# Kernel optimization log

Measured on AMD Instinct MI355X. Metric: run time of the kernel, lower is better.

## Reference

```python
import jax, jax.numpy as jnp
import numpy as np

B, H, D = 8, 2048, 2
K_COUPLE = 1.0
DT = 1.0
ALPHA_SCALE = 1.0


def setup_inputs() -> dict:
    key = jax.random.key(0)
    k1, k2, k3, k4, k5 = jax.random.split(key, 5)
    theta_prev = jax.random.normal(k1, (B, H, D), dtype=jnp.float32)
    gamma = jax.random.normal(k2, (B, H), dtype=jnp.float32)
    A = jax.random.uniform(k3, (B, H, H), dtype=jnp.float32)
    omega = jax.random.normal(k4, (H, D), dtype=jnp.float32) * 0.1
    kappa = jnp.ones((H, D), dtype=jnp.float32)
    direction_learner = jax.random.normal(k5, (H, H), dtype=jnp.float32) * 0.01
    return {"theta_prev": theta_prev, "gamma": gamma, "A": A,
            "omega": omega, "kappa": kappa, "direction_learner": direction_learner}


def reference(theta_prev, gamma, A, omega, kappa, direction_learner):
    b, h, d = theta_prev.shape
    # Symmetrized, positive lateral connectivity
    A_lat = 0.5 * (A + jnp.swapaxes(A, 1, 2))
    A_lat = jax.nn.relu(A_lat) + 1e-6  # [B,H,H]
    # OT surrogate: normalized cost, antisymmetric learned direction -> phase lag alpha
    cost = 1.0 / A_lat
    c_min = jnp.min(cost, axis=(1, 2), keepdims=True)
    c_max = jnp.max(cost, axis=(1, 2), keepdims=True)
    norm_cost = (cost - c_min) / (c_max - c_min + 1e-6)
    direction_mask = jnp.tanh(direction_learner - direction_learner.T)  # [H,H]
    alpha = (ALPHA_SCALE * direction_mask[None, :, :] * norm_cost)[..., None]  # [B,H,H,1]
    # Pairwise phase interaction: sum_j A_ij * sin(theta_j - theta_i - alpha_ij)
    theta_i = theta_prev[:, :, None, :]  # [B,H,1,D]
    theta_j = theta_prev[:, None, :, :]  # [B,1,H,D]
    phase_diff = theta_j - theta_i - alpha  # [B,H,H,D]
    interaction = jnp.sum(A_lat[..., None] * jnp.sin(phase_diff), axis=2)  # [B,H,D]
    coupling = (K_COUPLE / float(h)) * interaction
    drive = kappa * jnp.sin(gamma[..., None] - theta_prev)
    theta_dot = omega + coupling + drive
    return theta_prev + DT * theta_dot
```

## Files before the change

### kernel.cpp

```cpp
#include <hip/hip_runtime.h>
#include <hip/hip_fp16.h>

#define B 8
#define H 2048
#define D 2
#define HH (H*H)
#define TILE 64
#define NT (H/TILE)
#define NPAIR (NT*(NT+1)/2)
#define NJC 8
#define JC (H/NJC)
#define WJ (JC/4)
#define SUB 16
#define NSUB (WJ/SUB)
#define INV2PI 0.15915494309189535f

__device__ __forceinline__ float fsin(float x) { return __builtin_amdgcn_sinf(x * INV2PI); }
__device__ __forceinline__ float fcos(float x) { return __builtin_amdgcn_cosf(x * INV2PI); }


__global__ __launch_bounds__(256) void k_dmpre(
    const float* __restrict__ dl, __half* __restrict__ dm,
    const float* __restrict__ theta, const float* __restrict__ gamma,
    const float* __restrict__ omega, const float* __restrict__ kappa,
    float* __restrict__ out, float4* __restrict__ sc) {
    int ti = blockIdx.x, tj = blockIdx.y;
    int t = threadIdx.x, c = t & 63, r0 = t >> 6;
    __shared__ float l2[TILE][TILE + 1];

    float v[16];
    #pragma unroll
    for (int k = 0; k < 16; k++)
        v[k] = dl[(size_t)(tj * TILE + r0 + 4 * k) * H + ti * TILE + c];
    #pragma unroll
    for (int k = 0; k < 16; k++) l2[r0 + 4 * k][c] = v[k];
    __syncthreads();
    #pragma unroll
    for (int k = 0; k < 16; k++)
        v[k] = dl[(size_t)(ti * TILE + r0 + 4 * k) * H + tj * TILE + c];
    #pragma unroll
    for (int k = 0; k < 16; k++) {
        int il = r0 + 4 * k;
        float x = v[k] - l2[c][il];
        float x2 = x * x;
        float w = x * fmaf(x2, fmaf(x2, 0.13333334f, -0.33333334f), 1.0f);
        dm[(size_t)(ti * TILE + il) * H + tj * TILE + c] = __float2half(w);
    }

    int bid = blockIdx.y * NT + blockIdx.x;
    if (bid < (B * H) / 256) {
        int g = bid * 256 + t;
        int i = g & (H - 1);
        float th0 = theta[(size_t)g * 2 + 0];
        float th1 = theta[(size_t)g * 2 + 1];
        sc[g] = make_float4(fsin(th0), fcos(th0), fsin(th1), fcos(th1));
        float gm = gamma[g];
        out[(size_t)g * 2 + 0] = th0 + omega[i * 2 + 0] + kappa[i * 2 + 0] * fsin(gm - th0);
        out[(size_t)g * 2 + 1] = th1 + omega[i * 2 + 1] + kappa[i * 2 + 1] * fsin(gm - th1);
    }
}

__global__ __launch_bounds__(256) void k_minmax(const float* __restrict__ A,
                                                float* __restrict__ pmn,
                                                float* __restrict__ pmx) {
    int b = blockIdx.y;
    int tp = blockIdx.x;
    int pid = b * NPAIR + tp;
    int ti = 0;
    while (tp >= NT - ti) { tp -= NT - ti; ti++; }
    int tj = ti + tp;

    __shared__ float l2[TILE][TILE + 1];
    const float* Ab = A + (size_t)b * HH;
    int t = threadIdx.x;
    int c = t & 63, r0 = t >> 6;

    float v[16];
    #pragma unroll
    for (int k = 0; k < 16; k++)
        v[k] = Ab[(size_t)(tj * TILE + r0 + 4 * k) * H + ti * TILE + c];
    #pragma unroll
    for (int k = 0; k < 16; k++) l2[r0 + 4 * k][c] = v[k];
    __syncthreads();

    #pragma unroll
    for (int k = 0; k < 16; k++)
        v[k] = Ab[(size_t)(ti * TILE + r0 + 4 * k) * H + tj * TILE + c];

    float mn = 3.0e38f, mx = 0.f;
    #pragma unroll
    for (int k = 0; k < 16; k++) {
        int il = r0 + 4 * k;
        float s = fmaxf(0.5f * (v[k] + l2[c][il]), 0.f) + 1e-6f;
        mn = fminf(mn, s); mx = fmaxf(mx, s);
    }
    #pragma unroll
    for (int off = 32; off; off >>= 1) {
        mn = fminf(mn, __shfl_xor(mn, off));
        mx = fmaxf(mx, __shfl_xor(mx, off));
    }
    __shared__ float smn[4], smx[4];
    int wv = t >> 6, ln = t & 63;
    if (ln == 0) { smn[wv] = mn; smx[wv] = mx; }
    __syncthreads();
    if (t == 0) {
        for (int i = 1; i < 4; i++) { mn = fminf(mn, smn[i]); mx = fmaxf(mx, smx[i]); }
        pmn[pid] = mn;
        pmx[pid] = mx;
    }
}

__global__ __launch_bounds__(256) void k_mmred(const float* __restrict__ pmn,
                                               const float* __restrict__ pmx,
                                               float* __restrict__ mmf) {
    int b = blockIdx.x, t = threadIdx.x;
    float mn = 3.0e38f, mx = 0.f;
    for (int k = t; k < NPAIR; k += 256) {
        mn = fminf(mn, pmn[b * NPAIR + k]);
        mx = fmaxf(mx, pmx[b * NPAIR + k]);
    }
    #pragma unroll
    for (int off = 32; off; off >>= 1) {
        mn = fminf(mn, __shfl_xor(mn, off));
        mx = fmaxf(mx, __shfl_xor(mx, off));
    }
    __shared__ float smn[4], smx[4];
    int wv = t >> 6, ln = t & 63;
    if (ln == 0) { smn[wv] = mn; smx[wv] = mx; }
    __syncthreads();
    if (t == 0) {
        for (int i = 1; i < 4; i++) { mn = fminf(mn, smn[i]); mx = fmaxf(mx, smx[i]); }
        mmf[b * 2 + 0] = mn;
        mmf[b * 2 + 1] = mx;
    }
}

__global__ __launch_bounds__(256, 8) void k_main(
    const float* __restrict__ A, const __half* __restrict__ dm,
    const float4* __restrict__ sc, const float* __restrict__ mmf,
    float* __restrict__ out) {
    int it = blockIdx.x, jc = blockIdx.y, b = blockIdx.z;
    int t = threadIdx.x, w = t >> 6, ln = t & 63;
    int i0 = it * TILE;
    int i = i0 + ln;

    __shared__ float tile[4][SUB][TILE + 1];
    __shared__ float red[4][TILE][2];

    float amin = mmf[b * 2 + 0];
    float amax = mmf[b * 2 + 1];
    float cmin = 1.0f / amax, cmax = 1.0f / amin;
    float invr = 1.0f / (cmax - cmin + 1e-6f);
    float ncb = cmin * invr;

    const float* Ab = A + (size_t)b * HH;
    const float4* scb = sc + (size_t)b * H;
    float4 sci = scb[i];
    float si0 = sci.x, ci0 = sci.y, si1 = sci.z, ci1 = sci.w;
    float acc0 = 0.f, acc1 = 0.f;

    int jbase = jc * JC + w * WJ;
    int rr = ln >> 2, cc = (ln & 3) * 4;
    for (int st = 0; st < NSUB; st++) {
        int j0 = jbase + st * SUB;
        #pragma unroll
        for (int g = 0; g < 4; g++) {
            int r = rr + g * 16;
            float4 v = *(const float4*)(Ab + (size_t)(i0 + r) * H + j0 + cc);
            tile[w][cc + 0][r] = v.x;
            tile[w][cc + 1][r] = v.y;
            tile[w][cc + 2][r] = v.z;
            tile[w][cc + 3][r] = v.w;
        }
        #pragma unroll 2
        for (int jj = 0; jj < SUB; jj++) {
            int j = j0 + jj;
            float4 scj = scb[j];
            float aji = Ab[(size_t)j * H + i];
            float dmv = __half2float(dm[(size_t)j * H + i]);
            float aij = tile[w][jj][ln];
            float al = fmaxf(0.5f * (aij + aji), 0.f) + 1e-6f;
            float cost = __builtin_amdgcn_rcpf(al);
            float nc = fmaf(cost, invr, -ncb);
            float alpha = -dmv * nc;
            float a2 = alpha * alpha;
            float sa = alpha * fmaf(a2, -0.16666667f, 1.0f);
            float ca = fmaf(a2, -0.5f, 1.0f);
            float sd0 = fmaf(scj.x, ci0, -scj.y * si0);
            float cd0 = fmaf(scj.y, ci0,  scj.x * si0);
            acc0 = fmaf(al, fmaf(sd0, ca, -cd0 * sa), acc0);
            float sd1 = fmaf(scj.z, ci1, -scj.w * si1);
            float cd1 = fmaf(scj.w, ci1,  scj.z * si1);
            acc1 = fmaf(al, fmaf(sd1, ca, -cd1 * sa), acc1);
        }
    }

    red[w][ln][0] = acc0; red[w][ln][1] = acc1;
    __syncthreads();
    if (w == 0) {
        float r0s = red[0][ln][0] + red[1][ln][0] + red[2][ln][0] + red[3][ln][0];
        float r1s = red[0][ln][1] + red[1][ln][1] + red[2][ln][1] + red[3][ln][1];
        atomicAdd(&out[(size_t)(b * H + i) * 2 + 0], r0s * (1.0f / H));
        atomicAdd(&out[(size_t)(b * H + i) * 2 + 1], r1s * (1.0f / H));
    }
}


__global__ void k_init_fb(unsigned int* mm) {
    int t = threadIdx.x;
    if (t < B * 2) mm[t] = (t & 1) ? 0u : 0x7f800000u;
}

__global__ __launch_bounds__(256) void k_minmax_fb(const float* __restrict__ A,
                                                   unsigned int* __restrict__ mm) {
    int b = blockIdx.y;
    int tp = blockIdx.x;
    int ti = 0;
    while (tp >= NT - ti) { tp -= NT - ti; ti++; }
    int tj = ti + tp;

    __shared__ float l2[TILE][TILE + 1];
    const float* Ab = A + (size_t)b * HH;
    int t = threadIdx.x;
    int c = t & 63, r0 = t >> 6;

    #pragma unroll
    for (int k = 0; k < 16; k++)
        l2[r0 + 4 * k][c] = Ab[(size_t)(tj * TILE + r0 + 4 * k) * H + ti * TILE + c];
    __syncthreads();

    float mn = 3.0e38f, mx = 0.f;
    #pragma unroll
    for (int k = 0; k < 16; k++) {
        int il = r0 + 4 * k;
        float aij = Ab[(size_t)(ti * TILE + il) * H + tj * TILE + c];
        float v = fmaxf(0.5f * (aij + l2[c][il]), 0.f) + 1e-6f;
        mn = fminf(mn, v); mx = fmaxf(mx, v);
    }
    #pragma unroll
    for (int off = 32; off; off >>= 1) {
        mn = fminf(mn, __shfl_xor(mn, off));
        mx = fmaxf(mx, __shfl_xor(mx, off));
    }
    __shared__ float smn[4], smx[4];
    int wv = t >> 6, ln = t & 63;
    if (ln == 0) { smn[wv] = mn; smx[wv] = mx; }
    __syncthreads();
    if (t == 0) {
        for (int i = 1; i < 4; i++) { mn = fminf(mn, smn[i]); mx = fmaxf(mx, smx[i]); }
        atomicMin(&mm[b * 2 + 0], __float_as_uint(mn));
        atomicMax(&mm[b * 2 + 1], __float_as_uint(mx));
    }
}

__global__ __launch_bounds__(1024) void k_main_fb(
    const float* __restrict__ theta, const float* __restrict__ gamma,
    const float* __restrict__ A, const float* __restrict__ omega,
    const float* __restrict__ kappa, const float* __restrict__ dl,
    const unsigned int* __restrict__ mm, float* __restrict__ out) {
    int b = blockIdx.y;
    int i0 = blockIdx.x * TILE;
    int t = threadIdx.x;
    int w = t >> 6, ln = t & 63;

    __shared__ float aT[TILE][TILE + 1];
    __shared__ float dT[TILE][TILE + 1];
    __shared__ float thI[4][TILE];
    __shared__ float thJ[4][TILE];

    float amin = __uint_as_float(mm[b * 2 + 0]);
    float amax = __uint_as_float(mm[b * 2 + 1]);
    float cmin = 1.0f / amax, cmax = 1.0f / amin;
    float invr = 1.0f / (cmax - cmin + 1e-6f);

    if (t < 128) {
        int il = t & 63, d = t >> 6;
        float th = theta[(size_t)(b * H + i0 + il) * D + d];
        thI[d * 2 + 0][il] = fsin(th);
        thI[d * 2 + 1][il] = fcos(th);
    }
    __syncthreads();

    float si[4][2], ci[4][2];
    #pragma unroll
    for (int k = 0; k < 4; k++)
        #pragma unroll
        for (int d = 0; d < 2; d++) {
            si[k][d] = thI[d * 2 + 0][w * 4 + k];
            ci[k][d] = thI[d * 2 + 1][w * 4 + k];
        }

    float acc[4][2] = {};
    const float* Ab = A + (size_t)b * HH;

    for (int jt = 0; jt < NT; jt++) {
        int j0 = jt * TILE;
        __syncthreads();
        #pragma unroll
        for (int k = 0; k < 4; k++) {
            int r = w * 4 + k;
            aT[r][ln] = Ab[(size_t)(j0 + r) * H + i0 + ln];
            dT[r][ln] = dl[(size_t)(j0 + r) * H + i0 + ln];
        }
        if (t < 128) {
            int jl = t & 63, d = t >> 6;
            float th = theta[(size_t)(b * H + j0 + jl) * D + d];
            thJ[d * 2 + 0][jl] = fsin(th);
            thJ[d * 2 + 1][jl] = fcos(th);
        }
        __syncthreads();

        float sj0 = thJ[0][ln], cj0 = thJ[1][ln];
        float sj1 = thJ[2][ln], cj1 = thJ[3][ln];
        const float* arow = Ab + (size_t)(i0 + w * 4) * H + j0 + ln;
        const float* drow = dl + (size_t)(i0 + w * 4) * H + j0 + ln;
        #pragma unroll
        for (int k = 0; k < 4; k++) {
            float aij = arow[(size_t)k * H];
            float dij = drow[(size_t)k * H];
            float aji = aT[ln][w * 4 + k];
            float dji = dT[ln][w * 4 + k];
            float al = fmaxf(0.5f * (aij + aji), 0.f) + 1e-6f;
            float cost = __builtin_amdgcn_rcpf(al);
            float nc = (cost - cmin) * invr;
            float x = dij - dji;
            float x2 = x * x;
            float dmv = x * fmaf(x2, fmaf(x2, 0.13333334f, -0.33333334f), 1.0f);
            float alpha = dmv * nc;
            float sa = fsin(alpha), ca = fcos(alpha);
            {
                float sd = sj0 * ci[k][0] - cj0 * si[k][0];
                float cd = cj0 * ci[k][0] + sj0 * si[k][0];
                acc[k][0] = fmaf(al, sd * ca - cd * sa, acc[k][0]);
            }
            {
                float sd = sj1 * ci[k][1] - cj1 * si[k][1];
                float cd = cj1 * ci[k][1] + sj1 * si[k][1];
                acc[k][1] = fmaf(al, sd * ca - cd * sa, acc[k][1]);
            }
        }
    }

    #pragma unroll
    for (int k = 0; k < 4; k++)
        #pragma unroll
        for (int d = 0; d < 2; d++)
            #pragma unroll
            for (int off = 32; off; off >>= 1)
                acc[k][d] += __shfl_xor(acc[k][d], off);

    if (ln < 8) {
        int k = ln >> 1, d = ln & 1;
        int i = i0 + w * 4 + k;
        size_t idx = (size_t)(b * H + i) * D + d;
        float chosen = __shfl(acc[k][d], k * 2 + d);
        float th = theta[idx];
        float drv = kappa[i * D + d] * fsin(gamma[b * H + i] - th);
        out[idx] = th + (omega[i * D + d] + (1.0f / H) * chosen + drv);
    }
}


extern "C" void kernel_launch(void* const* d_in, const int* in_sizes, int n_in,
                              void* d_out, int out_size, void* d_ws, size_t ws_size,
                              hipStream_t stream) {
    const float* theta = (const float*)d_in[0];
    const float* gamma = (const float*)d_in[1];
    const float* A     = (const float*)d_in[2];
    const float* omega = (const float*)d_in[3];
    const float* kappa = (const float*)d_in[4];
    const float* dl    = (const float*)d_in[5];
    float* out = (float*)d_out;

    float* mmf = (float*)d_ws;
    float* pmn = (float*)((char*)d_ws + 1024);
    float* pmx = pmn + B * NPAIR;
    float4* sc = (float4*)((char*)d_ws + 65536);
    __half* dm = (__half*)((char*)d_ws + 65536 + (size_t)B * H * 16);
    size_t need = 65536 + (size_t)B * H * 16 + (size_t)HH * 2;

    if (ws_size >= need) {
        hipLaunchKernelGGL(k_dmpre, dim3(NT, NT), dim3(256), 0, stream,
                           dl, dm, theta, gamma, omega, kappa, out, sc);
        hipLaunchKernelGGL(k_minmax, dim3(NPAIR, B), dim3(256), 0, stream, A, pmn, pmx);
        hipLaunchKernelGGL(k_mmred, dim3(B), dim3(256), 0, stream, pmn, pmx, mmf);
        hipLaunchKernelGGL(k_main, dim3(NT, NJC, B), dim3(256), 0, stream,
                           A, dm, sc, mmf, out);
    } else {
        unsigned int* mm = (unsigned int*)d_ws;
        hipLaunchKernelGGL(k_init_fb, dim3(1), dim3(64), 0, stream, mm);
        hipLaunchKernelGGL(k_minmax_fb, dim3(NPAIR, B), dim3(256), 0, stream, A, mm);
        hipLaunchKernelGGL(k_main_fb, dim3(NT, B), dim3(1024), 0, stream,
                           theta, gamma, A, omega, kappa, dl, mm, out);
    }
}
```

Before: 277.2 us.

## Exploit pair symmetry with triangular tiles and bf16-staged lateral weights

A_lat is symmetric and the phase lag is antisymmetric, so each pair term contributes with opposite sign to i and j. The main kernel now walks only upper-triangular 64x64 tile pairs and adds row sums and negated column sums through atomics, halving the sin/weight evaluations. The min/max pass is fused into a staging kernel that reads A once and writes the symmetrized, relu'd weights in bf16 per tile pair. The direction mask is also stored per tile pair. This removes repeated full-precision reads of A in the main pass. The cost is extra atomics, per-row wavefront shuffle reductions, and reduced precision of A_lat from bf16 storage.

```diff
diff --git a/kernel.cpp b/kernel.cpp
--- a/kernel.cpp
+++ b/kernel.cpp
@@ -1,5 +1,6 @@
 #include <hip/hip_runtime.h>
 #include <hip/hip_fp16.h>
+#include <hip/hip_bf16.h>
 
 #define B 8
 #define H 2048
@@ -8,48 +9,92 @@
 #define TILE 64
 #define NT (H/TILE)
 #define NPAIR (NT*(NT+1)/2)
-#define NJC 8
-#define JC (H/NJC)
-#define WJ (JC/4)
-#define SUB 16
-#define NSUB (WJ/SUB)
 #define INV2PI 0.15915494309189535f
+#define INVH (1.0f/2048.0f)
 
 __device__ __forceinline__ float fsin(float x) { return __builtin_amdgcn_sinf(x * INV2PI); }
 __device__ __forceinline__ float fcos(float x) { return __builtin_amdgcn_cosf(x * INV2PI); }
 
-
-__global__ __launch_bounds__(256) void k_dmpre(
-    const float* __restrict__ dl, __half* __restrict__ dm,
+__device__ __forceinline__ void pair_decode(int tp, int& ti, int& tj) {
+    ti = 0;
+    while (tp >= NT - ti) { tp -= NT - ti; ti++; }
+    tj = ti + tp;
+}
+
+__global__ __launch_bounds__(256) void k_stage(
+    const float* __restrict__ A, const float* __restrict__ dl,
     const float* __restrict__ theta, const float* __restrict__ gamma,
     const float* __restrict__ omega, const float* __restrict__ kappa,
-    float* __restrict__ out, float4* __restrict__ sc) {
-    int ti = blockIdx.x, tj = blockIdx.y;
+    float* __restrict__ out, float4* __restrict__ sc,
+    __hip_bfloat16* __restrict__ alw, __half* __restrict__ dmw,
+    float* __restrict__ pmn, float* __restrict__ pmx) {
+    int pair = blockIdx.x, b = blockIdx.y;
+    int ti, tj; pair_decode(pair, ti, tj);
     int t = threadIdx.x, c = t & 63, r0 = t >> 6;
+
     __shared__ float l2[TILE][TILE + 1];
+    const float* Ab = A + (size_t)b * HH;
 
     float v[16];
     #pragma unroll
     for (int k = 0; k < 16; k++)
-        v[k] = dl[(size_t)(tj * TILE + r0 + 4 * k) * H + ti * TILE + c];
+        v[k] = Ab[(size_t)(tj * TILE + r0 + 4 * k) * H + ti * TILE + c];
     #pragma unroll
     for (int k = 0; k < 16; k++) l2[r0 + 4 * k][c] = v[k];
     __syncthreads();
     #pragma unroll
     for (int k = 0; k < 16; k++)
-        v[k] = dl[(size_t)(ti * TILE + r0 + 4 * k) * H + tj * TILE + c];
+        v[k] = Ab[(size_t)(ti * TILE + r0 + 4 * k) * H + tj * TILE + c];
+
+    __hip_bfloat16* alp = alw + ((size_t)b * NPAIR + pair) * (TILE * TILE);
+    float mn = 3.0e38f, mx = 0.f;
     #pragma unroll
     for (int k = 0; k < 16; k++) {
         int il = r0 + 4 * k;
-        float x = v[k] - l2[c][il];
-        float x2 = x * x;
-        float w = x * fmaf(x2, fmaf(x2, 0.13333334f, -0.33333334f), 1.0f);
-        dm[(size_t)(ti * TILE + il) * H + tj * TILE + c] = __float2half(w);
-    }
-
-    int bid = blockIdx.y * NT + blockIdx.x;
-    if (bid < (B * H) / 256) {
-        int g = bid * 256 + t;
+        float al = fmaxf(0.5f * (v[k] + l2[c][il]), 0.f) + 1e-6f;
+        mn = fminf(mn, al); mx = fmaxf(mx, al);
+        alp[il * TILE + c] = __float2bfloat16(al);
+    }
+    #pragma unroll
+    for (int off = 32; off; off >>= 1) {
+        mn = fminf(mn, __shfl_xor(mn, off));
+        mx = fmaxf(mx, __shfl_xor(mx, off));
+    }
+    __shared__ float smn[4], smx[4];
+    int wv = t >> 6, ln = t & 63;
+    if (ln == 0) { smn[wv] = mn; smx[wv] = mx; }
+    __syncthreads();
+    if (t == 0) {
+        for (int i = 1; i < 4; i++) { mn = fminf(mn, smn[i]); mx = fmaxf(mx, smx[i]); }
+        pmn[b * NPAIR + pair] = mn;
+        pmx[b * NPAIR + pair] = mx;
+    }
+
+    if (b == 0) {
+        __syncthreads();
+        float w2[16];
+        #pragma unroll
+        for (int k = 0; k < 16; k++)
+            w2[k] = dl[(size_t)(tj * TILE + r0 + 4 * k) * H + ti * TILE + c];
+        #pragma unroll
+        for (int k = 0; k < 16; k++) l2[r0 + 4 * k][c] = w2[k];
+        __syncthreads();
+        #pragma unroll
+        for (int k = 0; k < 16; k++)
+            w2[k] = dl[(size_t)(ti * TILE + r0 + 4 * k) * H + tj * TILE + c];
+        __half* dmp = dmw + (size_t)pair * (TILE * TILE);
+        #pragma unroll
+        for (int k = 0; k < 16; k++) {
+            int il = r0 + 4 * k;
+            float x = w2[k] - l2[c][il];
+            float x2 = x * x;
+            float dmv = x * fmaf(x2, fmaf(x2, 0.13333334f, -0.33333334f), 1.0f);
+            dmp[il * TILE + c] = __float2half(dmv);
+        }
+    }
+
+    if (b == 1 && pair < (B * H) / 256) {
+        int g = pair * 256 + t;
         int i = g & (H - 1);
         float th0 = theta[(size_t)g * 2 + 0];
         float th1 = theta[(size_t)g * 2 + 1];
@@ -57,56 +102,6 @@
         float gm = gamma[g];
         out[(size_t)g * 2 + 0] = th0 + omega[i * 2 + 0] + kappa[i * 2 + 0] * fsin(gm - th0);
         out[(size_t)g * 2 + 1] = th1 + omega[i * 2 + 1] + kappa[i * 2 + 1] * fsin(gm - th1);
-    }
-}
-
-__global__ __launch_bounds__(256) void k_minmax(const float* __restrict__ A,
-                                                float* __restrict__ pmn,
-                                                float* __restrict__ pmx) {
-    int b = blockIdx.y;
-    int tp = blockIdx.x;
-    int pid = b * NPAIR + tp;
-    int ti = 0;
-    while (tp >= NT - ti) { tp -= NT - ti; ti++; }
-    int tj = ti + tp;
-
-    __shared__ float l2[TILE][TILE + 1];
-    const float* Ab = A + (size_t)b * HH;
-    int t = threadIdx.x;
-    int c = t & 63, r0 = t >> 6;
-
-    float v[16];
-    #pragma unroll
-    for (int k = 0; k < 16; k++)
-        v[k] = Ab[(size_t)(tj * TILE + r0 + 4 * k) * H + ti * TILE + c];
-    #pragma unroll
-    for (int k = 0; k < 16; k++) l2[r0 + 4 * k][c] = v[k];
-    __syncthreads();
-
-    #pragma unroll
-    for (int k = 0; k < 16; k++)
-        v[k] = Ab[(size_t)(ti * TILE + r0 + 4 * k) * H + tj * TILE + c];
-
-    float mn = 3.0e38f, mx = 0.f;
-    #pragma unroll
-    for (int k = 0; k < 16; k++) {
-        int il = r0 + 4 * k;
-        float s = fmaxf(0.5f * (v[k] + l2[c][il]), 0.f) + 1e-6f;
-        mn = fminf(mn, s); mx = fmaxf(mx, s);
-    }
-    #pragma unroll
-    for (int off = 32; off; off >>= 1) {
-        mn = fminf(mn, __shfl_xor(mn, off));
-        mx = fmaxf(mx, __shfl_xor(mx, off));
-    }
-    __shared__ float smn[4], smx[4];
-    int wv = t >> 6, ln = t & 63;
-    if (ln == 0) { smn[wv] = mn; smx[wv] = mx; }
-    __syncthreads();
-    if (t == 0) {
-        for (int i = 1; i < 4; i++) { mn = fminf(mn, smn[i]); mx = fmaxf(mx, smx[i]); }
-        pmn[pid] = mn;
-        pmx[pid] = mx;
     }
 }
 
@@ -135,16 +130,16 @@
     }
 }
 
-__global__ __launch_bounds__(256, 8) void k_main(
-    const float* __restrict__ A, const __half* __restrict__ dm,
+__global__ __launch_bounds__(256) void k_main(
+    const __hip_bfloat16* __restrict__ alw, const __half* __restrict__ dmw,
     const float4* __restrict__ sc, const float* __restrict__ mmf,
     float* __restrict__ out) {
-    int it = blockIdx.x, jc = blockIdx.y, b = blockIdx.z;
+    int pair = blockIdx.x, b = blockIdx.y;
+    int ti, tj; pair_decode(pair, ti, tj);
+    bool diag = (ti == tj);
     int t = threadIdx.x, w = t >> 6, ln = t & 63;
-    int i0 = it * TILE;
-    int i = i0 + ln;
-
-    __shared__ float tile[4][SUB][TILE + 1];
+
+    __shared__ float4 ldssc[TILE];
     __shared__ float red[4][TILE][2];
 
     float amin = mmf[b * 2 + 0];
@@ -153,55 +148,66 @@
     float invr = 1.0f / (cmax - cmin + 1e-6f);
     float ncb = cmin * invr;
 
-    const float* Ab = A + (size_t)b * HH;
     const float4* scb = sc + (size_t)b * H;
-    float4 sci = scb[i];
-    float si0 = sci.x, ci0 = sci.y, si1 = sci.z, ci1 = sci.w;
-    float acc0 = 0.f, acc1 = 0.f;
-
-    int jbase = jc * JC + w * WJ;
-    int rr = ln >> 2, cc = (ln & 3) * 4;
-    for (int st = 0; st < NSUB; st++) {
-        int j0 = jbase + st * SUB;
-        #pragma unroll
-        for (int g = 0; g < 4; g++) {
-            int r = rr + g * 16;
-            float4 v = *(const float4*)(Ab + (size_t)(i0 + r) * H + j0 + cc);
-            tile[w][cc + 0][r] = v.x;
-            tile[w][cc + 1][r] = v.y;
-            tile[w][cc + 2][r] = v.z;
-            tile[w][cc + 3][r] = v.w;
-        }
-        #pragma unroll 2
-        for (int jj = 0; jj < SUB; jj++) {
-            int j = j0 + jj;
-            float4 scj = scb[j];
-            float aji = Ab[(size_t)j * H + i];
-            float dmv = __half2float(dm[(size_t)j * H + i]);
-            float aij = tile[w][jj][ln];
-            float al = fmaxf(0.5f * (aij + aji), 0.f) + 1e-6f;
-            float cost = __builtin_amdgcn_rcpf(al);
-            float nc = fmaf(cost, invr, -ncb);
-            float alpha = -dmv * nc;
-            float a2 = alpha * alpha;
-            float sa = alpha * fmaf(a2, -0.16666667f, 1.0f);
-            float ca = fmaf(a2, -0.5f, 1.0f);
-            float sd0 = fmaf(scj.x, ci0, -scj.y * si0);
-            float cd0 = fmaf(scj.y, ci0,  scj.x * si0);
-            acc0 = fmaf(al, fmaf(sd0, ca, -cd0 * sa), acc0);
-            float sd1 = fmaf(scj.z, ci1, -scj.w * si1);
-            float cd1 = fmaf(scj.w, ci1,  scj.z * si1);
-            acc1 = fmaf(al, fmaf(sd1, ca, -cd1 * sa), acc1);
-        }
-    }
-
-    red[w][ln][0] = acc0; red[w][ln][1] = acc1;
-    __syncthreads();
-    if (w == 0) {
-        float r0s = red[0][ln][0] + red[1][ln][0] + red[2][ln][0] + red[3][ln][0];
-        float r1s = red[0][ln][1] + red[1][ln][1] + red[2][ln][1] + red[3][ln][1];
-        atomicAdd(&out[(size_t)(b * H + i) * 2 + 0], r0s * (1.0f / H));
-        atomicAdd(&out[(size_t)(b * H + i) * 2 + 1], r1s * (1.0f / H));
+    if (t < TILE) ldssc[t] = scb[ti * TILE + t];
+
+    int j = tj * TILE + ln;
+    float4 scj = scb[j];
+    float sj0 = scj.x, cj0 = scj.y, sj1 = scj.z, cj1 = scj.w;
+    __syncthreads();
+
+    const __hip_bfloat16* alp = alw + ((size_t)b * NPAIR + pair) * (TILE * TILE);
+    const __half* dmp = dmw + (size_t)pair * (TILE * TILE);
+
+    float accj0 = 0.f, accj1 = 0.f;
+    float rs = 0.f;
+
+    #pragma unroll
+    for (int k = 0; k < 16; k++) {
+        int il = w * 16 + k;
+        float4 sciv = ldssc[il];
+        float si0 = sciv.x, ci0 = sciv.y, si1 = sciv.z, ci1 = sciv.w;
+
+        float al = __bfloat162float(alp[il * TILE + ln]);
+        float dmv = __half2float(dmp[il * TILE + ln]);
+        float cost = __builtin_amdgcn_rcpf(al);
+        float nc = fmaf(cost, invr, -ncb);
+        float alpha = dmv * nc;
+        float a2 = alpha * alpha;
+        float sa = alpha * fmaf(a2, -0.16666667f, 1.0f);
+        float ca = fmaf(a2, -0.5f, 1.0f);
+        float sd0 = fmaf(sj0, ci0, -cj0 * si0);
+        float cd0 = fmaf(cj0, ci0,  sj0 * si0);
+        float c0 = al * fmaf(sd0, ca, -cd0 * sa);
+        float sd1 = fmaf(sj1, ci1, -cj1 * si1);
+        float cd1 = fmaf(cj1, ci1,  sj1 * si1);
+        float c1 = al * fmaf(sd1, ca, -cd1 * sa);
+
+        accj0 -= c0;
+        accj1 -= c1;
+
+        float s0 = c0, s1 = c1;
+        #pragma unroll
+        for (int off = 32; off; off >>= 1) {
+            s0 += __shfl_xor(s0, off);
+            s1 += __shfl_xor(s1, off);
+        }
+        if (ln == 2 * k)     rs = s0;
+        if (ln == 2 * k + 1) rs = s1;
+    }
+
+    if (ln < 32) {
+        int k = ln >> 1, d = ln & 1;
+        int i = ti * TILE + w * 16 + k;
+        atomicAdd(&out[(size_t)(b * H + i) * 2 + d], rs * INVH);
+    }
+
+    red[w][ln][0] = accj0; red[w][ln][1] = accj1;
+    __syncthreads();
+    if (!diag && t < 128) {
+        int jl = t >> 1, d = t & 1;
+        float cs = red[0][jl][d] + red[1][jl][d] + red[2][jl][d] + red[3][jl][d];
+        atomicAdd(&out[(size_t)(b * H + tj * TILE + jl) * 2 + d], cs * INVH);
     }
 }
 
@@ -215,9 +221,7 @@
                                                    unsigned int* __restrict__ mm) {
     int b = blockIdx.y;
     int tp = blockIdx.x;
-    int ti = 0;
-    while (tp >= NT - ti) { tp -= NT - ti; ti++; }
-    int tj = ti + tp;
+    int ti, tj; pair_decode(tp, ti, tj);
 
     __shared__ float l2[TILE][TILE + 1];
     const float* Ab = A + (size_t)b * HH;
@@ -376,16 +380,18 @@
     float* pmn = (float*)((char*)d_ws + 1024);
     float* pmx = pmn + B * NPAIR;
     float4* sc = (float4*)((char*)d_ws + 65536);
-    __half* dm = (__half*)((char*)d_ws + 65536 + (size_t)B * H * 16);
-    size_t need = 65536 + (size_t)B * H * 16 + (size_t)HH * 2;
+    __half* dmw = (__half*)((char*)d_ws + 65536 + 262144);
+    __hip_bfloat16* alw = (__hip_bfloat16*)((char*)d_ws + 65536 + 262144
+                          + (size_t)NPAIR * TILE * TILE * 2);
+    size_t need = 65536 + 262144 + (size_t)NPAIR * TILE * TILE * 2
+                + (size_t)B * NPAIR * TILE * TILE * 2;
 
     if (ws_size >= need) {
-        hipLaunchKernelGGL(k_dmpre, dim3(NT, NT), dim3(256), 0, stream,
-                           dl, dm, theta, gamma, omega, kappa, out, sc);
-        hipLaunchKernelGGL(k_minmax, dim3(NPAIR, B), dim3(256), 0, stream, A, pmn, pmx);
+        hipLaunchKernelGGL(k_stage, dim3(NPAIR, B), dim3(256), 0, stream,
+                           A, dl, theta, gamma, omega, kappa, out, sc, alw, dmw, pmn, pmx);
         hipLaunchKernelGGL(k_mmred, dim3(B), dim3(256), 0, stream, pmn, pmx, mmf);
-        hipLaunchKernelGGL(k_main, dim3(NT, NJC, B), dim3(256), 0, stream,
-                           A, dm, sc, mmf, out);
+        hipLaunchKernelGGL(k_main, dim3(NPAIR, B), dim3(256), 0, stream,
+                           alw, dmw, sc, mmf, out);
     } else {
         unsigned int* mm = (unsigned int*)d_ws;
         hipLaunchKernelGGL(k_init_fb, dim3(1), dim3(64), 0, stream, mm);
```

Result: faster. 259.2 us (-6.5%).
